# Performance work log

Measured on AMD Instinct MI355X. Metric: run time of the kernel, lower is better.

The kernel has to match this reference:

```python
import jax, jax.numpy as jnp
import numpy as np

BLOCK_DIMS = (128, 256)
EPS = 1e-8


def l2norm(x, axis=-1):
    norm = jnp.sqrt(jnp.sum(x * x, axis=axis, keepdims=True)) + EPS
    return x / norm


def setup_inputs() -> dict:
    key = jax.random.key(0)
    k1, k2 = jax.random.split(key)
    img_emb = jax.random.normal(k1, (2048, 1024), dtype=jnp.float32)
    cap_emb = jax.random.normal(k2, (2048, 1024), dtype=jnp.float32)
    return {"img_emb": img_emb, "cap_emb": cap_emb}


def reference(img_emb, cap_emb):
    # Global l2norm of captions first (as in original forward)
    cap_emb = l2norm(cap_emb, -1)
    n_img, img_dim = img_emb.shape
    n_cap, cap_dim = cap_emb.shape
    sims = jnp.zeros((n_img, n_cap), dtype=img_emb.dtype)
    for block_dim in BLOCK_DIMS:
        v = img_dim // block_dim  # number of image blocks
        t = cap_dim // block_dim  # number of caption blocks
        # chunk along last dim + stack == reshape to [n, blocks, block_dim]
        img_blk = l2norm(img_emb.reshape(n_img, v, block_dim), -1)
        cap_blk = l2norm(cap_emb.reshape(n_cap, t, block_dim), -1)
        # [a, b, v, t] block-cosine similarities
        logits = jnp.einsum('avc,btc->abvt', img_blk, cap_blk)
        # max over image blocks v, then sum over caption blocks t
        sims = sims + jnp.max(logits, axis=2).sum(axis=-1)
    return sims
```

## Files before the change

### kernel.cpp

```cpp
#include <hip/hip_runtime.h>
#include <hip/hip_bf16.h>

typedef short short8 __attribute__((ext_vector_type(8)));
typedef float f32x4 __attribute__((ext_vector_type(4)));

#define EPSF 1e-8f
#define NROWS 16384

__device__ __forceinline__ unsigned short f2bf(float f) {
  __hip_bfloat16 h = __float2bfloat16(f);
  return *reinterpret_cast<unsigned short*>(&h);
}

template <int CTRL>
__device__ __forceinline__ float dppf(float x) {
  return __builtin_bit_cast(
      float, __builtin_amdgcn_update_dpp(0, __builtin_bit_cast(int, x), CTRL,
                                         0xF, 0xF, true));
}
#define DPP_XOR1 0xB1
#define DPP_XOR2 0x4E
#define DPP_P4 0x12C

__device__ __forceinline__ float swz16(float x) {
  return __builtin_bit_cast(
      float, __builtin_amdgcn_ds_swizzle(__builtin_bit_cast(int, x), 0x401F));
}

__global__ __launch_bounds__(256) void prep_kernel(
    const float* __restrict__ img, const float* __restrict__ cap,
    unsigned short* __restrict__ Ahat, unsigned short* __restrict__ Bhat,
    float* __restrict__ fa_e, float* __restrict__ fa_o,
    float* __restrict__ fb_e, float* __restrict__ fb_o)
{
  int tid = threadIdx.x;
  int row = blockIdx.x & 2047;
  int isCap = blockIdx.x >> 11;
  const float* src = isCap ? cap : img;
  unsigned short* dstHat = isCap ? Bhat : Ahat;

  float4 v = reinterpret_cast<const float4*>(src + (size_t)row * 1024)[tid];
  float ss = v.x * v.x + v.y * v.y + v.z * v.z + v.w * v.w;
  ss += __shfl_xor(ss, 1);
  ss += __shfl_xor(ss, 2);
  ss += __shfl_xor(ss, 4);
  ss += __shfl_xor(ss, 8);
  ss += __shfl_xor(ss, 16);
  float s128 = ss;
  float s256 = s128 + __shfl_xor(s128, 32);

  __shared__ float wsum[4];
  if ((tid & 63) == 0) wsum[tid >> 6] = s256;
  __syncthreads();
  float rowsum = wsum[0] + wsum[1] + wsum[2] + wsum[3];
  float rn = sqrtf(rowsum) + EPSF;

  float scale;
  if (isCap) scale = 1.0f / (sqrtf(s128) + EPSF * rn);
  else       scale = 1.0f / (sqrtf(s128) + EPSF);

  unsigned int lo = (unsigned int)f2bf(v.x * scale) | ((unsigned int)f2bf(v.y * scale) << 16);
  unsigned int hi = (unsigned int)f2bf(v.z * scale) | ((unsigned int)f2bf(v.w * scale) << 16);

  int j = tid >> 5;
  int rh = row * 8 + j;
  int s = (tid & 31) >> 1;
  uint2* p = reinterpret_cast<uint2*>(
      (char*)dstHat + ((size_t)s * NROWS + rh) * 16 + ((tid & 1) << 3));
  *p = make_uint2(lo, hi);

  int l63 = tid & 63;
  if (l63 == 0 || l63 == 32) {
    float n128, n256;
    if (isCap) { n128 = sqrtf(s128) / rn + EPSF; n256 = sqrtf(s256) / rn + EPSF; }
    else       { n128 = sqrtf(s128) + EPSF;      n256 = sqrtf(s256) + EPSF; }
    float f = n128 / n256;
    int v256 = tid >> 6;
    float* dst;
    if (l63 == 0) dst = isCap ? fb_e : fa_e;
    else          dst = isCap ? fb_o : fa_o;
    dst[row * 4 + v256] = f;
  }
}

__global__ __launch_bounds__(256) void sims_kernel(
    const unsigned short* __restrict__ Ahat, const unsigned short* __restrict__ Bhat,
    const float* __restrict__ fa_e, const float* __restrict__ fa_o,
    const float* __restrict__ fb_e, const float* __restrict__ fb_o,
    float* __restrict__ out)
{
  __shared__ float outLds[256];
  int tid = threadIdx.x;
  int lane = tid & 63;
  int w = tid >> 6;

  int bx = blockIdx.x;
  int x = bx & 7;
  int l = bx >> 3;
  int tm = l >> 4;
  int tn = (x << 4) | (l & 15);
  int m0 = tm * 128;
  int n0 = tn * 128;

  int wr = (w >> 1) * 64;
  int wc = (w & 1) * 64;
  int rl = lane & 15;
  int g = lane >> 4;

  const char* Ab = (const char*)Ahat;
  const char* Bb = (const char*)Bhat;

  f32x4 acc[4][4] = {};

#pragma unroll
  for (int kt = 0; kt < 4; ++kt) {
    int s = kt * 4 + g;
    const char* As = Ab + ((size_t)s * NROWS + m0 + wr + rl) * 16;
    const char* Bs = Bb + ((size_t)s * NROWS + n0 + wc + rl) * 16;
    short8 av[4], bv[4];
#pragma unroll
    for (int f = 0; f < 4; ++f) {
      av[f] = *reinterpret_cast<const short8*>(As + f * (16 * 16));
      bv[f] = *reinterpret_cast<const short8*>(Bs + f * (16 * 16));
    }
#pragma unroll
    for (int fm = 0; fm < 4; ++fm)
#pragma unroll
      for (int fn = 0; fn < 4; ++fn)
        acc[fm][fn] = __builtin_amdgcn_mfma_f32_16x16x32_bf16(av[fm], bv[fn], acc[fm][fn], 0, 0, 0);
  }

  float fbe[4], fbo[4];
  int colBase = n0 + wc + rl;
#pragma unroll
  for (int fn = 0; fn < 4; ++fn) {
    int nb = (colBase + fn * 16) >> 1;
    fbe[fn] = fb_e[nb];
    fbo[fn] = fb_o[nb];
  }

  bool writer = ((lane & 7) == 0) && ((g & 1) == 0);

#pragma unroll
  for (int fm = 0; fm < 4; ++fm) {
    int rBase = m0 + wr + fm * 16 + 4 * g;
    int vi = rBase >> 1;
    float fae0 = fa_e[vi], fao0 = fa_o[vi];
    float fae1 = fa_e[vi + 1], fao1 = fa_o[vi + 1];
#pragma unroll
    for (int fn = 0; fn < 4; ++fn) {
      f32x4 a = acc[fm][fn];

      float mm = fmaxf(fmaxf(a[0], a[1]), fmaxf(a[2], a[3]));
      mm = fmaxf(mm, swz16(mm));
      float y = mm;
      y += dppf<DPP_XOR1>(y);
      y += dppf<DPP_XOR2>(y);
      y += dppf<DPP_P4>(y);

      float s1 = dppf<DPP_XOR1>(a[1]);
      float s3 = dppf<DPP_XOR1>(a[3]);
      float qa = a[0] * (fae0 * fbe[fn]) + s1 * (fao0 * fbo[fn]);
      float qb = a[2] * (fae1 * fbe[fn]) + s3 * (fao1 * fbo[fn]);
      float qm = fmaxf(qa, qb);
      qm = fmaxf(qm, swz16(qm));
      float z = qm;
      z += dppf<DPP_XOR2>(z);
      z += dppf<DPP_P4>(z);

      if (writer) {
        int pi = (wr >> 3) + fm * 2 + (g >> 1);
        int pj = (wc >> 3) + fn * 2 + (rl >> 3);
        outLds[pi * 16 + pj] = y + z;
      }
    }
  }

  __syncthreads();
  int pr = tid >> 4, pc = tid & 15;
  out[(size_t)(tm * 16 + pr) * 2048 + (tn * 16 + pc)] = outLds[tid];
}

extern "C" void kernel_launch(void* const* d_in, const int* in_sizes, int n_in,
                              void* d_out, int out_size, void* d_ws, size_t ws_size,
                              hipStream_t stream) {
  const float* img = (const float*)d_in[0];
  const float* cap = (const float*)d_in[1];
  float* out = (float*)d_out;

  char* ws = (char*)d_ws;
  unsigned short* Ahat = (unsigned short*)ws;
  unsigned short* Bhat = (unsigned short*)(ws + (size_t)4 * 1024 * 1024);
  float* fa_e = (float*)(ws + (size_t)8 * 1024 * 1024);
  float* fa_o = fa_e + 8192;
  float* fb_e = fa_o + 8192;
  float* fb_o = fb_e + 8192;

  prep_kernel<<<4096, 256, 0, stream>>>(img, cap, Ahat, Bhat, fa_e, fa_o, fb_e, fb_o);
  sims_kernel<<<16384, 256, 0, stream>>>(Ahat, Bhat, fa_e, fa_o, fb_e, fb_o, out);
}
```

Measured before the change: 186.6 us.

## Coalesce prep stores via LDS, interleave scale factors, merge DPP reductions

The prep kernel now stages its bf16 outputs in shared memory so each block writes contiguous 16-byte chunks in a transposed order instead of scattered 8-byte stores. The even/odd scale-factor arrays are interleaved, so the sims kernel loads them as float2/float4 vectors, and the fb loads are issued before the MFMA loop. In the epilogue the y and z reductions are combined before the shared DPP XOR2/P4 steps, update_dpp is replaced by mov_dpp, and sims_kernel gains a launch_bounds occupancy hint of 4. The extra LDS round trip and barrier in prep add some latency, and the occupancy hint may push register use down.

```diff
diff --git a/kernel.cpp b/kernel.cpp
--- a/kernel.cpp
+++ b/kernel.cpp
@@ -13,10 +13,9 @@
 }
 
 template <int CTRL>
-__device__ __forceinline__ float dppf(float x) {
+__device__ __forceinline__ float dmov(float x) {
   return __builtin_bit_cast(
-      float, __builtin_amdgcn_update_dpp(0, __builtin_bit_cast(int, x), CTRL,
-                                         0xF, 0xF, true));
+      float, __builtin_amdgcn_mov_dpp(__builtin_bit_cast(int, x), CTRL, 0xF, 0xF, false));
 }
 #define DPP_XOR1 0xB1
 #define DPP_XOR2 0x4E
@@ -30,9 +29,10 @@
 __global__ __launch_bounds__(256) void prep_kernel(
     const float* __restrict__ img, const float* __restrict__ cap,
     unsigned short* __restrict__ Ahat, unsigned short* __restrict__ Bhat,
-    float* __restrict__ fa_e, float* __restrict__ fa_o,
-    float* __restrict__ fb_e, float* __restrict__ fb_o)
+    float* __restrict__ fa, float* __restrict__ fb)
 {
+  __shared__ float wsum[4];
+  __shared__ uint2 lds2[16 * 18];
   int tid = threadIdx.x;
   int row = blockIdx.x & 2047;
   int isCap = blockIdx.x >> 11;
@@ -49,7 +49,6 @@
   float s128 = ss;
   float s256 = s128 + __shfl_xor(s128, 32);
 
-  __shared__ float wsum[4];
   if ((tid & 63) == 0) wsum[tid >> 6] = s256;
   __syncthreads();
   float rowsum = wsum[0] + wsum[1] + wsum[2] + wsum[3];
@@ -63,11 +62,9 @@
   unsigned int hi = (unsigned int)f2bf(v.z * scale) | ((unsigned int)f2bf(v.w * scale) << 16);
 
   int j = tid >> 5;
-  int rh = row * 8 + j;
   int s = (tid & 31) >> 1;
-  uint2* p = reinterpret_cast<uint2*>(
-      (char*)dstHat + ((size_t)s * NROWS + rh) * 16 + ((tid & 1) << 3));
-  *p = make_uint2(lo, hi);
+  int half = tid & 1;
+  lds2[s * 18 + j * 2 + half] = make_uint2(lo, hi);
 
   int l63 = tid & 63;
   if (l63 == 0 || l63 == 32) {
@@ -76,17 +73,20 @@
     else       { n128 = sqrtf(s128) + EPSF;      n256 = sqrtf(s256) + EPSF; }
     float f = n128 / n256;
     int v256 = tid >> 6;
-    float* dst;
-    if (l63 == 0) dst = isCap ? fb_e : fa_e;
-    else          dst = isCap ? fb_o : fa_o;
-    dst[row * 4 + v256] = f;
+    float* dst = isCap ? fb : fa;
+    dst[(row * 4 + v256) * 2 + (l63 == 32 ? 1 : 0)] = f;
   }
+  __syncthreads();
+
+  int s2 = tid >> 4, j2 = (tid & 15) >> 1, h2 = tid & 1;
+  uint2 val = lds2[s2 * 18 + j2 * 2 + h2];
+  *reinterpret_cast<uint2*>(
+      (char*)dstHat + ((size_t)s2 * NROWS + row * 8 + j2) * 16 + h2 * 8) = val;
 }
 
-__global__ __launch_bounds__(256) void sims_kernel(
+__global__ __launch_bounds__(256, 4) void sims_kernel(
     const unsigned short* __restrict__ Ahat, const unsigned short* __restrict__ Bhat,
-    const float* __restrict__ fa_e, const float* __restrict__ fa_o,
-    const float* __restrict__ fb_e, const float* __restrict__ fb_o,
+    const float* __restrict__ fa, const float* __restrict__ fb,
     float* __restrict__ out)
 {
   __shared__ float outLds[256];
@@ -107,21 +107,28 @@
   int rl = lane & 15;
   int g = lane >> 4;
 
-  const char* Ab = (const char*)Ahat;
-  const char* Bb = (const char*)Bhat;
+  unsigned vA = (unsigned)g * (NROWS * 16u) + (unsigned)(m0 + wr + rl) * 16u;
+  unsigned vB = (unsigned)g * (NROWS * 16u) + (unsigned)(n0 + wc + rl) * 16u;
+  const char* Abase = (const char*)Ahat;
+  const char* Bbase = (const char*)Bhat;
+
+  float2 fbv[4];
+  int colBase = n0 + wc + rl;
+#pragma unroll
+  for (int fn = 0; fn < 4; ++fn)
+    fbv[fn] = *reinterpret_cast<const float2*>(fb + ((colBase + fn * 16) >> 1) * 2);
 
   f32x4 acc[4][4] = {};
 
 #pragma unroll
   for (int kt = 0; kt < 4; ++kt) {
-    int s = kt * 4 + g;
-    const char* As = Ab + ((size_t)s * NROWS + m0 + wr + rl) * 16;
-    const char* Bs = Bb + ((size_t)s * NROWS + n0 + wc + rl) * 16;
+    const char* Ak = Abase + (size_t)kt * (4u * NROWS * 16u);
+    const char* Bk = Bbase + (size_t)kt * (4u * NROWS * 16u);
     short8 av[4], bv[4];
 #pragma unroll
     for (int f = 0; f < 4; ++f) {
-      av[f] = *reinterpret_cast<const short8*>(As + f * (16 * 16));
-      bv[f] = *reinterpret_cast<const short8*>(Bs + f * (16 * 16));
+      av[f] = *reinterpret_cast<const short8*>(Ak + vA + f * 256);
+      bv[f] = *reinterpret_cast<const short8*>(Bk + vB + f * 256);
     }
 #pragma unroll
     for (int fm = 0; fm < 4; ++fm)
@@ -130,49 +137,34 @@
         acc[fm][fn] = __builtin_amdgcn_mfma_f32_16x16x32_bf16(av[fm], bv[fn], acc[fm][fn], 0, 0, 0);
   }
 
-  float fbe[4], fbo[4];
-  int colBase = n0 + wc + rl;
-#pragma unroll
-  for (int fn = 0; fn < 4; ++fn) {
-    int nb = (colBase + fn * 16) >> 1;
-    fbe[fn] = fb_e[nb];
-    fbo[fn] = fb_o[nb];
-  }
-
   bool writer = ((lane & 7) == 0) && ((g & 1) == 0);
+  int pBase = ((wr >> 3) + (g >> 1)) * 16 + (wc >> 3) + (rl >> 3);
 
 #pragma unroll
   for (int fm = 0; fm < 4; ++fm) {
     int rBase = m0 + wr + fm * 16 + 4 * g;
     int vi = rBase >> 1;
-    float fae0 = fa_e[vi], fao0 = fa_o[vi];
-    float fae1 = fa_e[vi + 1], fao1 = fa_o[vi + 1];
+    float4 fav = *reinterpret_cast<const float4*>(fa + vi * 2);
 #pragma unroll
     for (int fn = 0; fn < 4; ++fn) {
       f32x4 a = acc[fm][fn];
 
       float mm = fmaxf(fmaxf(a[0], a[1]), fmaxf(a[2], a[3]));
-      mm = fmaxf(mm, swz16(mm));
-      float y = mm;
-      y += dppf<DPP_XOR1>(y);
-      y += dppf<DPP_XOR2>(y);
-      y += dppf<DPP_P4>(y);
+      float m8 = fmaxf(mm, swz16(mm));
+      float u = m8 + dmov<DPP_XOR1>(m8);
 
-      float s1 = dppf<DPP_XOR1>(a[1]);
-      float s3 = dppf<DPP_XOR1>(a[3]);
-      float qa = a[0] * (fae0 * fbe[fn]) + s1 * (fao0 * fbo[fn]);
-      float qb = a[2] * (fae1 * fbe[fn]) + s3 * (fao1 * fbo[fn]);
+      float s1 = dmov<DPP_XOR1>(a[1]);
+      float s3 = dmov<DPP_XOR1>(a[3]);
+      float qa = a[0] * (fav.x * fbv[fn].x) + s1 * (fav.y * fbv[fn].y);
+      float qb = a[2] * (fav.z * fbv[fn].x) + s3 * (fav.w * fbv[fn].y);
       float qm = fmaxf(qa, qb);
       qm = fmaxf(qm, swz16(qm));
-      float z = qm;
-      z += dppf<DPP_XOR2>(z);
-      z += dppf<DPP_P4>(z);
 
-      if (writer) {
-        int pi = (wr >> 3) + fm * 2 + (g >> 1);
-        int pj = (wc >> 3) + fn * 2 + (rl >> 3);
-        outLds[pi * 16 + pj] = y + z;
-      }
+      float wv = u + qm;
+      wv += dmov<DPP_XOR2>(wv);
+      wv += dmov<DPP_P4>(wv);
+
+      if (writer) outLds[pBase + fm * 32 + fn * 2] = wv;
     }
   }
 
@@ -191,11 +183,9 @@
   char* ws = (char*)d_ws;
   unsigned short* Ahat = (unsigned short*)ws;
   unsigned short* Bhat = (unsigned short*)(ws + (size_t)4 * 1024 * 1024);
-  float* fa_e = (float*)(ws + (size_t)8 * 1024 * 1024);
-  float* fa_o = fa_e + 8192;
-  float* fb_e = fa_o + 8192;
-  float* fb_o = fb_e + 8192;
+  float* fa = (float*)(ws + (size_t)8 * 1024 * 1024);
+  float* fb = fa + 2048 * 4 * 2;
 
-  prep_kernel<<<4096, 256, 0, stream>>>(img, cap, Ahat, Bhat, fa_e, fa_o, fb_e, fb_o);
-  sims_kernel<<<16384, 256, 0, stream>>>(Ahat, Bhat, fa_e, fa_o, fb_e, fb_o, out);
+  prep_kernel<<<4096, 256, 0, stream>>>(img, cap, Ahat, Bhat, fa, fb);
+  sims_kernel<<<16384, 256, 0, stream>>>(Ahat, Bhat, fa, fb, out);
 }
```

Result: faster. 166.1 us (-11.0%).
